# Kernel optimization log

Hardware: AMD Instinct MI355X
Metric: run time of the kernel (lower is better)

## Reference

```python
import jax, jax.numpy as jnp
import numpy as np

D_MODEL = 1024
H = 16
D = D_MODEL // H  # 64 per head
D_FF = 4096
LN_EPS = 1e-5


def layer_norm(x, gamma, beta):
    mu = jnp.mean(x, axis=-1, keepdims=True)
    var = jnp.mean(jnp.square(x - mu), axis=-1, keepdims=True)
    return (x - mu) * jax.lax.rsqrt(var + LN_EPS) * gamma + beta


def setup_inputs() -> dict:
    key = jax.random.key(0)
    ks = jax.random.split(key, 12)
    s = 1.0 / np.sqrt(D_MODEL)
    sf = 1.0 / np.sqrt(D_FF)
    return {
        "x": jax.random.normal(ks[0], (2, 2048, D_MODEL), jnp.float32),
        "src_mask": 0,
        "w_q": jax.random.normal(ks[1], (D_MODEL, D_MODEL), jnp.float32) * s,
        "w_k": jax.random.normal(ks[2], (D_MODEL, D_MODEL), jnp.float32) * s,
        "w_v": jax.random.normal(ks[3], (D_MODEL, D_MODEL), jnp.float32) * s,
        "w_0": jax.random.normal(ks[4], (D_MODEL, D_MODEL), jnp.float32) * s,
        "b_0": jnp.zeros((D_MODEL,), jnp.float32),
        "w_1": jax.random.normal(ks[5], (D_MODEL, D_FF), jnp.float32) * s,
        "b_1": jnp.zeros((D_FF,), jnp.float32),
        "w_2": jax.random.normal(ks[6], (D_FF, D_MODEL), jnp.float32) * sf,
        "b_2": jnp.zeros((D_MODEL,), jnp.float32),
        "g_1": jnp.ones((D_MODEL,), jnp.float32),
        "be_1": jnp.zeros((D_MODEL,), jnp.float32),
        "g_2": jnp.ones((D_MODEL,), jnp.float32),
        "be_2": jnp.zeros((D_MODEL,), jnp.float32),
    }


def reference(x, src_mask, w_q, w_k, w_v, w_0, b_0, w_1, b_1, w_2, b_2, g_1, be_1, g_2, be_2):
    N, S, _ = x.shape
    # --- pre-LN self-attention branch ---
    x_n = layer_norm(x, g_1, be_1)
    q = (x_n @ w_q).reshape(N, S, H, D).transpose(0, 2, 1, 3)  # [N,H,S,D]
    k = (x_n @ w_k).reshape(N, S, H, D).transpose(0, 2, 1, 3)
    v = (x_n @ w_v).reshape(N, S, H, D).transpose(0, 2, 1, 3)
    scores = jnp.einsum('nhqd,nhkd->nhqk', q, k) / np.sqrt(D)
    # src_mask == 0 (falsy) in the original -> no masking applied
    attn = jax.nn.softmax(scores, axis=-1)
    out = jnp.einsum('nhqk,nhkd->nhqd', attn, v)
    out = out.transpose(0, 2, 1, 3).reshape(N, S, H * D)
    attn_out = out @ w_0 + b_0
    x = x + attn_out  # dropout is identity in eval
    # --- pre-LN feedforward branch ---
    x_n = layer_norm(x, g_2, be_2)
    ff = jax.nn.relu(x_n @ w_1 + b_1) @ w_2 + b_2
    return x + ff
```

## Files before the change

kernel.cpp:

```cpp
#include <hip/hip_runtime.h>

typedef __bf16 bf16x8 __attribute__((ext_vector_type(8)));
typedef float f32x4 __attribute__((ext_vector_type(4)));
typedef unsigned short u16x8 __attribute__((ext_vector_type(8)));
typedef unsigned short u16x4 __attribute__((ext_vector_type(4)));

__device__ __forceinline__ unsigned short f2bf_bits(float f) {
  unsigned u = __float_as_uint(f);
  return (unsigned short)((u + 0x7FFFu + ((u >> 16) & 1u)) >> 16);
}

__device__ __forceinline__ float exp2_amd(float x) {
  return __builtin_amdgcn_exp2f(x);
}

__device__ __forceinline__ unsigned cvt_pk_bf16(float a, float b) {
  unsigned r;
  asm("v_cvt_pk_bf16_f32 %0, %1, %2" : "=v"(r) : "v"(a), "v"(b));
  return r;
}

__device__ __forceinline__ void gload16(const void* g, void* l) {
  __builtin_amdgcn_global_load_lds(
      (const __attribute__((address_space(1))) unsigned int*)g,
      (__attribute__((address_space(3))) unsigned int*)l, 16, 0, 0);
}

__global__ __launch_bounds__(256) void wconv_t(const float* __restrict__ src,
                                               unsigned short* __restrict__ dst,
                                               int R, int C) {
  __shared__ float tile[32][33];
  const int tx = threadIdx.x & 31, ty = threadIdx.x >> 5;
  const size_t c0 = (size_t)blockIdx.x * 32, r0 = (size_t)blockIdx.y * 32;
#pragma unroll
  for (int i = 0; i < 4; i++)
    tile[ty + i * 8][tx] = src[(r0 + ty + i * 8) * C + c0 + tx];
  __syncthreads();
#pragma unroll
  for (int i = 0; i < 4; i++) {
    int c = ty + i * 8;
    dst[(c0 + c) * R + r0 + tx] = f2bf_bits(tile[tx][c]);
  }
}

__global__ __launch_bounds__(256) void ln_k(const float* __restrict__ x,
                                            const float* __restrict__ g,
                                            const float* __restrict__ be,
                                            unsigned short* __restrict__ o) {
  const int row = blockIdx.x, tid = threadIdx.x;
  const float4 v = ((const float4*)(x + (size_t)row * 1024))[tid];
  float s = v.x + v.y + v.z + v.w;
  float s2 = v.x * v.x + v.y * v.y + v.z * v.z + v.w * v.w;
#pragma unroll
  for (int m = 1; m < 64; m <<= 1) {
    s += __shfl_xor(s, m);
    s2 += __shfl_xor(s2, m);
  }
  __shared__ float red[8];
  const int w = tid >> 6;
  if ((tid & 63) == 0) { red[w] = s; red[4 + w] = s2; }
  __syncthreads();
  s = red[0] + red[1] + red[2] + red[3];
  s2 = red[4] + red[5] + red[6] + red[7];
  const float mu = s * (1.f / 1024.f);
  const float rs_ = rsqrtf(s2 * (1.f / 1024.f) - mu * mu + 1e-5f);
  const float4 gg = ((const float4*)g)[tid];
  const float4 bb = ((const float4*)be)[tid];
  u16x4 pack;
  pack.x = f2bf_bits((v.x - mu) * rs_ * gg.x + bb.x);
  pack.y = f2bf_bits((v.y - mu) * rs_ * gg.y + bb.y);
  pack.z = f2bf_bits((v.z - mu) * rs_ * gg.z + bb.z);
  pack.w = f2bf_bits((v.w - mu) * rs_ * gg.w + bb.w);
  *(u16x4*)(o + (size_t)row * 1024 + tid * 4) = pack;
}

template <int EPI>
__global__ __launch_bounds__(256) void gemm_bt(
    const unsigned short* __restrict__ A, const unsigned short* __restrict__ Bt,
    const float* __restrict__ bias, const float* __restrict__ res,
    void* __restrict__ Cv, int M, int N, int K) {
  __shared__ __align__(16) unsigned short As[128 * 64];
  __shared__ __align__(16) unsigned short Bs[128 * 64];
  const int tid = threadIdx.x, lane = tid & 63, w = tid >> 6;
  const int lo = lane & 15, hi = lane >> 4;
  const int l8 = lane >> 3, l7 = lane & 7;
  const int scol = ((l7 ^ l8) << 3);
  const size_t rowBase = (size_t)blockIdx.y * 128;
  const size_t colBase = (size_t)blockIdx.x * 128;
  f32x4 acc[4][4];
#pragma unroll
  for (int i = 0; i < 4; i++)
#pragma unroll
    for (int j = 0; j < 4; j++) acc[i][j] = (f32x4){0.f, 0.f, 0.f, 0.f};
  const int wr = (w >> 1) * 64, wc = (w & 1) * 64;
  const unsigned short* aSrc = A + (rowBase + (size_t)w * 32 + l8) * K + scol;
  const unsigned short* bSrc = Bt + (colBase + (size_t)w * 32 + l8) * K + scol;
  for (int kb = 0; kb < K; kb += 64) {
    __syncthreads();
#pragma unroll
    for (int c = 0; c < 4; c++) {
      gload16(aSrc + (size_t)c * 8 * K + kb, &As[(w * 4 + c) * 512]);
      gload16(bSrc + (size_t)c * 8 * K + kb, &Bs[(w * 4 + c) * 512]);
    }
    __syncthreads();
#pragma unroll
    for (int ks = 0; ks < 2; ks++) {
      bf16x8 af[4], bfr[4];
      const int kbyte = ks * 64 + (hi << 4);
#pragma unroll
      for (int i = 0; i < 4; i++) {
        const int ar = wr + i * 16 + lo;
        af[i] = *(const bf16x8*)((const char*)As + ar * 128 + (kbyte ^ ((ar & 7) << 4)));
        const int br = wc + i * 16 + lo;
        bfr[i] = *(const bf16x8*)((const char*)Bs + br * 128 + (kbyte ^ ((br & 7) << 4)));
      }
#pragma unroll
      for (int i = 0; i < 4; i++)
#pragma unroll
        for (int j = 0; j < 4; j++)
          acc[i][j] = __builtin_amdgcn_mfma_f32_16x16x32_bf16(af[i], bfr[j], acc[i][j], 0, 0, 0);
    }
  }
#pragma unroll
  for (int i = 0; i < 4; i++) {
#pragma unroll
    for (int r = 0; r < 4; r++) {
      const size_t row = rowBase + wr + i * 16 + hi * 4 + r;
#pragma unroll
      for (int j = 0; j < 4; j++) {
        const size_t col = colBase + wc + j * 16 + lo;
        float v = acc[i][j][r];
        if (EPI >= 1) v += bias[col];
        if (EPI == 1) {
          ((float*)Cv)[row * N + col] = v + res[row * N + col];
        } else if (EPI == 2) {
          ((unsigned short*)Cv)[row * N + col] = f2bf_bits(fmaxf(v, 0.f));
        } else {
          ((unsigned short*)Cv)[row * N + col] = f2bf_bits(v);
        }
      }
    }
  }
}

__global__ __launch_bounds__(256) void attn_k(const unsigned short* __restrict__ Q,
                                              const unsigned short* __restrict__ K,
                                              const unsigned short* __restrict__ V,
                                              unsigned short* __restrict__ O) {
  __shared__ __align__(16) unsigned short Ks[2][64 * 64];
  __shared__ __align__(16) unsigned short Vt[2][64 * 64];
  const int tid = threadIdx.x, lane = tid & 63, w = tid >> 6;
  const int lo = lane & 15, hi = lane >> 4;
  const int l8 = lane >> 3, l7 = lane & 7;
  const int scol = ((l7 ^ l8) << 3);
  const int h = blockIdx.y, n = blockIdx.z;
  const size_t tRow0 = (size_t)n * 2048;
  const int colBase = h * 64;
  const int LD = 3072;
  const float SC = 0.125f * 1.44269504f;

  const unsigned short* qrow = Q + (tRow0 + blockIdx.x * 64 + w * 16 + lo) * LD + colBase;
  const bf16x8 qf0 = *(const bf16x8*)(qrow + hi * 8);
  const bf16x8 qf1 = *(const bf16x8*)(qrow + 32 + hi * 8);
  float m2 = -1e30f, l_r = 0.f;
  f32x4 oacc[4];
#pragma unroll
  for (int d = 0; d < 4; d++) oacc[d] = (f32x4){0.f, 0.f, 0.f, 0.f};

  const int vkv = tid & 63, vdg = tid >> 6;
  const unsigned short* vbase = V + (tRow0 + vkv) * LD + colBase + vdg * 16;
  const unsigned short* kbase = K + (tRow0 + (size_t)w * 16 + l8) * LD + colBase + scol;

  u16x8 v0 = *(const u16x8*)(vbase);
  u16x8 v1 = *(const u16x8*)(vbase + 8);
#pragma unroll
  for (int c = 0; c < 2; c++)
    gload16(kbase + (size_t)c * 8 * LD, &Ks[0][(w * 2 + c) * 512]);
  {
    char* vt = (char*)Vt[0];
#pragma unroll
    for (int j = 0; j < 8; j++) {
      *(unsigned short*)(vt + (vdg * 16 + j) * 128 + ((vkv * 2) ^ (j << 4))) = v0[j];
      *(unsigned short*)(vt + (vdg * 16 + 8 + j) * 128 + ((vkv * 2) ^ (j << 4))) = v1[j];
    }
  }
  __syncthreads();

  for (int t = 0; t < 32; ++t) {
    const int cur = t & 1;
    if (t < 31) {
      v0 = *(const u16x8*)(vbase + (size_t)(t + 1) * 64 * LD);
      v1 = *(const u16x8*)(vbase + (size_t)(t + 1) * 64 * LD + 8);
#pragma unroll
      for (int c = 0; c < 2; c++)
        gload16(kbase + ((size_t)(t + 1) * 64 + c * 8) * LD, &Ks[cur ^ 1][(w * 2 + c) * 512]);
    }
    f32x4 s[4];
    const char* ksb = (const char*)Ks[cur];
    __builtin_amdgcn_s_setprio(1);
#pragma unroll
    for (int f = 0; f < 4; f++) {
      const int kr = f * 16 + lo;
      const bf16x8 b0 = *(const bf16x8*)(ksb + kr * 128 + ((hi * 16) ^ ((kr & 7) << 4)));
      const bf16x8 b1 = *(const bf16x8*)(ksb + kr * 128 + ((64 + hi * 16) ^ ((kr & 7) << 4)));
      s[f] = __builtin_amdgcn_mfma_f32_16x16x32_bf16(b0, qf0, (f32x4){0.f, 0.f, 0.f, 0.f}, 0, 0, 0);
      s[f] = __builtin_amdgcn_mfma_f32_16x16x32_bf16(b1, qf1, s[f], 0, 0, 0);
    }
    __builtin_amdgcn_s_setprio(0);
    float mx = fmaxf(fmaxf(fmaxf(s[0][0], s[0][1]), fmaxf(s[0][2], s[0][3])),
                     fmaxf(fmaxf(s[1][0], s[1][1]), fmaxf(s[1][2], s[1][3])));
    mx = fmaxf(mx, fmaxf(fmaxf(fmaxf(s[2][0], s[2][1]), fmaxf(s[2][2], s[2][3])),
                         fmaxf(fmaxf(s[3][0], s[3][1]), fmaxf(s[3][2], s[3][3]))));
    mx = fmaxf(mx, __shfl_xor(mx, 16));
    mx = fmaxf(mx, __shfl_xor(mx, 32));
    const float mx2v = mx * SC;
    if (__any(mx2v > m2 + 8.f)) {
      const float mn = fmaxf(m2, mx2v);
      const float al = exp2_amd(m2 - mn);
      l_r *= al;
      m2 = mn;
#pragma unroll
      for (int r = 0; r < 4; r++) {
        const float alr = __shfl(al, hi * 4 + r);
#pragma unroll
        for (int d = 0; d < 4; d++) oacc[d][r] *= alr;
      }
    }
    float p[4][4];
    float lsum = 0.f;
#pragma unroll
    for (int f = 0; f < 4; f++)
#pragma unroll
      for (int r = 0; r < 4; r++) {
        p[f][r] = exp2_amd(fmaf(s[f][r], SC, -m2));
        lsum += p[f][r];
      }
    l_r += lsum;
    unsigned W2[4][2];
#pragma unroll
    for (int f = 0; f < 4; f++) {
      W2[f][0] = cvt_pk_bf16(p[f][0], p[f][1]);
      W2[f][1] = cvt_pk_bf16(p[f][2], p[f][3]);
    }
    __builtin_amdgcn_s_setprio(1);
#pragma unroll
    for (int ks = 0; ks < 2; ks++) {
      unsigned wa[2], wb[2];
#pragma unroll
      for (int hh = 0; hh < 2; hh++) {
        unsigned X = W2[ks * 2][hh], Y = W2[ks * 2 + 1][hh];
        asm("v_permlane32_swap_b32 %0, %1" : "+v"(X), "+v"(Y));
        const unsigned Bx = __shfl_xor((int)Y, 16);
        const unsigned Ax = __shfl_xor((int)X, 16);
        wa[hh] = (hi & 1) ? Bx : X;
        wb[hh] = (hi & 1) ? Y : Ax;
      }
      union { unsigned u[4]; bf16x8 v; } apu;
      apu.u[0] = wa[0]; apu.u[1] = wa[1]; apu.u[2] = wb[0]; apu.u[3] = wb[1];
      const int kbyte = ks * 64 + (hi << 4);
#pragma unroll
      for (int d = 0; d < 4; d++) {
        const int dr = d * 16 + lo;
        const bf16x8 bv = *(const bf16x8*)((const char*)Vt[cur] + dr * 128 + (kbyte ^ ((dr & 7) << 4)));
        oacc[d] = __builtin_amdgcn_mfma_f32_16x16x32_bf16(apu.v, bv, oacc[d], 0, 0, 0);
      }
    }
    __builtin_amdgcn_s_setprio(0);
    if (t < 31) {
      char* vt = (char*)Vt[cur ^ 1];
#pragma unroll
      for (int j = 0; j < 8; j++) {
        *(unsigned short*)(vt + (vdg * 16 + j) * 128 + ((vkv * 2) ^ (j << 4))) = v0[j];
        *(unsigned short*)(vt + (vdg * 16 + 8 + j) * 128 + ((vkv * 2) ^ (j << 4))) = v1[j];
      }
    }
    __syncthreads();
  }
  float l = l_r;
  l += __shfl_xor(l, 16);
  l += __shfl_xor(l, 32);
  const float inv = 1.f / l;
#pragma unroll
  for (int r = 0; r < 4; r++) {
    const float invr = __shfl(inv, hi * 4 + r);
    const size_t row = tRow0 + blockIdx.x * 64 + w * 16 + hi * 4 + r;
#pragma unroll
    for (int d = 0; d < 4; d++)
      O[row * 1024 + colBase + d * 16 + lo] = f2bf_bits(oacc[d][r] * invr);
  }
}

extern "C" void kernel_launch(void* const* d_in, const int* in_sizes, int n_in,
                              void* d_out, int out_size, void* d_ws, size_t ws_size,
                              hipStream_t stream) {
  (void)in_sizes; (void)n_in; (void)out_size; (void)ws_size;
  const float* x   = (const float*)d_in[0];
  const float* w_q = (const float*)d_in[2];
  const float* w_k = (const float*)d_in[3];
  const float* w_v = (const float*)d_in[4];
  const float* w_0 = (const float*)d_in[5];
  const float* b_0 = (const float*)d_in[6];
  const float* w_1 = (const float*)d_in[7];
  const float* b_1 = (const float*)d_in[8];
  const float* w_2 = (const float*)d_in[9];
  const float* b_2 = (const float*)d_in[10];
  const float* g_1 = (const float*)d_in[11];
  const float* be_1 = (const float*)d_in[12];
  const float* g_2 = (const float*)d_in[13];
  const float* be_2 = (const float*)d_in[14];

  char* ws = (char*)d_ws;
  size_t off = 0;
  auto alloc = [&](size_t bytes) {
    void* p = ws + off;
    off += (bytes + 255) & ~(size_t)255;
    return p;
  };
  const size_t MB = 1024 * 1024;
  unsigned short* wt_q = (unsigned short*)alloc(2 * MB);
  unsigned short* wt_k = (unsigned short*)alloc(2 * MB);
  unsigned short* wt_v = (unsigned short*)alloc(2 * MB);
  unsigned short* wt_0 = (unsigned short*)alloc(2 * MB);
  unsigned short* wt_1 = (unsigned short*)alloc(8 * MB);
  unsigned short* wt_2 = (unsigned short*)alloc(8 * MB);
  unsigned short* xn   = (unsigned short*)alloc(8 * MB);
  unsigned short* qkv  = (unsigned short*)alloc(24 * MB);
  unsigned short* aO   = (unsigned short*)alloc(8 * MB);
  float*          x1f  = (float*)alloc(16 * MB);
  unsigned short* ff1  = (unsigned short*)alloc(32 * MB);

  wconv_t<<<dim3(32, 32), 256, 0, stream>>>(w_q, wt_q, 1024, 1024);
  wconv_t<<<dim3(32, 32), 256, 0, stream>>>(w_k, wt_k, 1024, 1024);
  wconv_t<<<dim3(32, 32), 256, 0, stream>>>(w_v, wt_v, 1024, 1024);
  wconv_t<<<dim3(32, 32), 256, 0, stream>>>(w_0, wt_0, 1024, 1024);
  wconv_t<<<dim3(128, 32), 256, 0, stream>>>(w_1, wt_1, 1024, 4096);
  wconv_t<<<dim3(32, 128), 256, 0, stream>>>(w_2, wt_2, 4096, 1024);

  ln_k<<<4096, 256, 0, stream>>>(x, g_1, be_1, xn);
  gemm_bt<0><<<dim3(24, 32), 256, 0, stream>>>(xn, wt_q, nullptr, nullptr, qkv, 4096, 3072, 1024);
  attn_k<<<dim3(32, 16, 2), 256, 0, stream>>>(qkv, qkv + 1024, qkv + 2048, aO);
  gemm_bt<1><<<dim3(8, 32), 256, 0, stream>>>(aO, wt_0, b_0, x, x1f, 4096, 1024, 1024);
  ln_k<<<4096, 256, 0, stream>>>(x1f, g_2, be_2, xn);
  gemm_bt<2><<<dim3(32, 32), 256, 0, stream>>>(xn, wt_1, b_1, nullptr, ff1, 4096, 4096, 1024);
  gemm_bt<1><<<dim3(8, 32), 256, 0, stream>>>(ff1, wt_2, b_2, x1f, (float*)d_out, 4096, 1024, 4096);
}
```

Baseline: 301.9 us.

## Double-buffer GEMM LDS tiles with async prefetch and XCD-aware block remap

Turns the bf16 GEMM mainloop into a two-stage LDS ping-pong that prefetches tile t+2 via global_load_lds while tile t is consumed, with explicit vmcnt waits and barriers replacing the load-then-compute pattern. It also remaps block IDs in groups of 8 so neighbouring tiles land on the same XCD for L2 reuse, and raises wave priority during the MFMA section. This doubles LDS use to 64KB per block, which can lower occupancy, and relies on hand-counted vmcnt values being correct.

```diff
diff --git a/kernel.cpp b/kernel.cpp
--- a/kernel.cpp
+++ b/kernel.cpp
@@ -79,14 +79,18 @@
     const unsigned short* __restrict__ A, const unsigned short* __restrict__ Bt,
     const float* __restrict__ bias, const float* __restrict__ res,
     void* __restrict__ Cv, int M, int N, int K) {
-  __shared__ __align__(16) unsigned short As[128 * 64];
-  __shared__ __align__(16) unsigned short Bs[128 * 64];
+  __shared__ __align__(16) unsigned short As[2][128 * 64];
+  __shared__ __align__(16) unsigned short Bs[2][128 * 64];
   const int tid = threadIdx.x, lane = tid & 63, w = tid >> 6;
   const int lo = lane & 15, hi = lane >> 4;
   const int l8 = lane >> 3, l7 = lane & 7;
   const int scol = ((l7 ^ l8) << 3);
-  const size_t rowBase = (size_t)blockIdx.y * 128;
-  const size_t colBase = (size_t)blockIdx.x * 128;
+  const int nwg = gridDim.x * gridDim.y;
+  int bid = blockIdx.y * gridDim.x + blockIdx.x;
+  if ((nwg & 7) == 0) bid = (bid & 7) * (nwg >> 3) + (bid >> 3);
+  const int bx = bid % gridDim.x, by = bid / gridDim.x;
+  const size_t rowBase = (size_t)by * 128;
+  const size_t colBase = (size_t)bx * 128;
   f32x4 acc[4][4];
 #pragma unroll
   for (int i = 0; i < 4; i++)
@@ -95,14 +99,27 @@
   const int wr = (w >> 1) * 64, wc = (w & 1) * 64;
   const unsigned short* aSrc = A + (rowBase + (size_t)w * 32 + l8) * K + scol;
   const unsigned short* bSrc = Bt + (colBase + (size_t)w * 32 + l8) * K + scol;
-  for (int kb = 0; kb < K; kb += 64) {
-    __syncthreads();
+
+  const int NT = K >> 6;
+  auto stage = [&](int t, int buf) {
+    const int kb = t << 6;
 #pragma unroll
     for (int c = 0; c < 4; c++) {
-      gload16(aSrc + (size_t)c * 8 * K + kb, &As[(w * 4 + c) * 512]);
-      gload16(bSrc + (size_t)c * 8 * K + kb, &Bs[(w * 4 + c) * 512]);
-    }
-    __syncthreads();
+      gload16(aSrc + (size_t)c * 8 * K + kb, &As[buf][(w * 4 + c) * 512]);
+      gload16(bSrc + (size_t)c * 8 * K + kb, &Bs[buf][(w * 4 + c) * 512]);
+    }
+  };
+
+  stage(0, 0);
+  stage(1, 1);
+  asm volatile("s_waitcnt vmcnt(8)" ::: "memory");
+  __builtin_amdgcn_s_barrier();
+
+  for (int t = 0; t < NT; ++t) {
+    const int cur = t & 1;
+    const char* asb = (const char*)As[cur];
+    const char* bsb = (const char*)Bs[cur];
+    __builtin_amdgcn_s_setprio(1);
 #pragma unroll
     for (int ks = 0; ks < 2; ks++) {
       bf16x8 af[4], bfr[4];
@@ -110,9 +127,9 @@
 #pragma unroll
       for (int i = 0; i < 4; i++) {
         const int ar = wr + i * 16 + lo;
-        af[i] = *(const bf16x8*)((const char*)As + ar * 128 + (kbyte ^ ((ar & 7) << 4)));
+        af[i] = *(const bf16x8*)(asb + ar * 128 + (kbyte ^ ((ar & 7) << 4)));
         const int br = wc + i * 16 + lo;
-        bfr[i] = *(const bf16x8*)((const char*)Bs + br * 128 + (kbyte ^ ((br & 7) << 4)));
+        bfr[i] = *(const bf16x8*)(bsb + br * 128 + (kbyte ^ ((br & 7) << 4)));
       }
 #pragma unroll
       for (int i = 0; i < 4; i++)
@@ -120,7 +137,18 @@
         for (int j = 0; j < 4; j++)
           acc[i][j] = __builtin_amdgcn_mfma_f32_16x16x32_bf16(af[i], bfr[j], acc[i][j], 0, 0, 0);
     }
-  }
+    __builtin_amdgcn_s_setprio(0);
+    asm volatile("s_waitcnt lgkmcnt(0)" ::: "memory");
+    __builtin_amdgcn_s_barrier();
+    if (t + 2 < NT) {
+      stage(t + 2, cur);
+      asm volatile("s_waitcnt vmcnt(8)" ::: "memory");
+    } else {
+      asm volatile("s_waitcnt vmcnt(0)" ::: "memory");
+    }
+    __builtin_amdgcn_s_barrier();
+  }
+
 #pragma unroll
   for (int i = 0; i < 4; i++) {
 #pragma unroll
```

Measured after the change: 284.8 us. -5.7%, faster.
